# Performance work log

Hardware: AMD Instinct MI355X
Metric: run time of the kernel (lower is better)

Reference implementation:

```python
import jax, jax.numpy as jnp
import numpy as np

B, T = 8192, 2048


def setup_inputs() -> dict:
    key = jax.random.key(0)
    u = jax.random.normal(key, (B, T, 1), dtype=jnp.float32)
    return {
        "u": u,
        "dt": jnp.float32(0.01),
        "m": jnp.float32(1.0),
        "c": jnp.float32(0.1),
        "k": jnp.float32(2.0),
        "in_mean": jnp.float32(0.5),
        "in_std": jnp.float32(2.0),
        "out_mean": jnp.float32(0.0),
        "out_std": jnp.float32(1.5),
    }


def reference(u, dt, m, c, k, in_mean, in_std, out_mean, out_std):
    # u: (B, T, 1) scaled forcing signal; state: (B, 2) = [position, velocity]
    Bsz = u.shape[0]
    u_seq = jnp.transpose(u[..., 0])  # (T, B) for lax.scan over time
    state0 = jnp.zeros((Bsz, 2), dtype=u.dtype)

    def step(state, u_t):
        # in_s.inverse_transform: unscale input
        u_p = u_t * in_std + in_mean  # (B,)
        x, v = state[:, 0], state[:, 1]
        # prior(state, u_p): mass-spring-damper derivative [dx, dv]
        acc = (u_p - c * v - k * x) / m
        new_state = state + dt * jnp.stack([v, acc], axis=1)  # Euler step
        # prior.ay on the UPDATED state (matches torch: state updated first)
        ay = (u_p - c * new_state[:, 1] - k * new_state[:, 0]) / m
        # out_s.transform: scale output
        y = (ay - out_mean) / out_std  # (B,)
        return new_state, y

    state_T, ys = jax.lax.scan(step, state0, u_seq)  # ys: (T, B)
    return jnp.transpose(ys), state_T  # (B, T), (B, 2)
```

## Files before the change

kernel.cpp:

```cpp
#include <hip/hip_runtime.h>

#define TT 2048
#define LP 32

__device__ __forceinline__ float b2f(unsigned short h) {
    union { unsigned int u; float f; } x; x.u = ((unsigned int)h) << 16; return x.f;
}
__device__ __forceinline__ unsigned short f2b(float f) {
    union { float f; unsigned int u; } x; x.f = f;
    unsigned int r = x.u + 0x7fffu + ((x.u >> 16) & 1u);
    return (unsigned short)(r >> 16);
}
__device__ __forceinline__ float ldsc(const void* p, bool bf) {
    return bf ? b2f(*(const unsigned short*)p) : *(const float*)p;
}

__global__ __launch_bounds__(256, 4) void phys_scan(
    const void* __restrict__ u_in,
    const void* __restrict__ p_dt, const void* __restrict__ p_m,
    const void* __restrict__ p_c,  const void* __restrict__ p_k,
    const void* __restrict__ p_im, const void* __restrict__ p_is,
    const void* __restrict__ p_om, const void* __restrict__ p_os,
    void* __restrict__ out, int rows)
{
    const int lane = threadIdx.x & 63;
    const int b = blockIdx.x * 4 + (threadIdx.x >> 6);
    if (b >= rows) return;

    const bool bf = (((const unsigned short*)p_m)[0] != 0);

    const float dt = ldsc(p_dt, bf);
    const float mm = ldsc(p_m,  bf);
    const float cc = ldsc(p_c,  bf);
    const float kk = ldsc(p_k,  bf);
    const float im = ldsc(p_im, bf);
    const float is = ldsc(p_is, bf);
    const float om = ldsc(p_om, bf);
    const float os = ldsc(p_os, bf);

    const float inv_m  = 1.0f / mm;
    const float inv_os = 1.0f / os;
    const float a21 = -dt * kk * inv_m;
    const float a22 = 1.0f - dt * cc * inv_m;
    const float dtm = dt * inv_m;

    const size_t base = (size_t)b * TT + (size_t)lane * LP;

    float uf[LP];
    if (bf) {
        const uint4* p = (const uint4*)((const unsigned short*)u_in + base);
        #pragma unroll
        for (int i = 0; i < 4; i++) {
            uint4 w = p[i];
            unsigned int ws[4] = {w.x, w.y, w.z, w.w};
            #pragma unroll
            for (int j = 0; j < 4; j++) {
                uf[i*8 + j*2 + 0] = b2f((unsigned short)(ws[j] & 0xffffu));
                uf[i*8 + j*2 + 1] = b2f((unsigned short)(ws[j] >> 16));
            }
        }
    } else {
        const float4* p = (const float4*)((const float*)u_in + base);
        #pragma unroll
        for (int i = 0; i < 8; i++) {
            float4 w = p[i];
            uf[i*4+0]=w.x; uf[i*4+1]=w.y; uf[i*4+2]=w.z; uf[i*4+3]=w.w;
        }
    }

    float px = 0.f, pv = 0.f;
    #pragma unroll
    for (int i = 0; i < LP; i++) {
        float up = uf[i] * is + im;
        uf[i] = up;
        float nx = px + dt * pv;
        float nv = a21 * px + a22 * pv + dtm * up;
        px = nx; pv = nv;
    }

    float m00 = 1.f, m01 = dt, m10 = a21, m11 = a22;
    #pragma unroll
    for (int i = 0; i < 5; i++) {
        float t00 = m00*m00 + m01*m10;
        float t01 = m00*m01 + m01*m11;
        float t10 = m10*m00 + m11*m10;
        float t11 = m10*m01 + m11*m11;
        m00=t00; m01=t01; m10=t10; m11=t11;
    }

    #pragma unroll
    for (int o = 1; o < 64; o <<= 1) {
        float rx = __shfl_up(px, o, 64);
        float rv = __shfl_up(pv, o, 64);
        if (lane >= o) {
            px = m00*rx + m01*rv + px;
            pv = m10*rx + m11*rv + pv;
        }
        if (o < 32) {
            float t00 = m00*m00 + m01*m10;
            float t01 = m00*m01 + m01*m11;
            float t10 = m10*m00 + m11*m10;
            float t11 = m10*m01 + m11*m11;
            m00=t00; m01=t01; m10=t10; m11=t11;
        }
    }

    float ex = __shfl_up(px, 1, 64);
    float ev = __shfl_up(pv, 1, 64);
    if (lane == 0) { ex = 0.f; ev = 0.f; }

    float x = ex, v = ev;
    #pragma unroll
    for (int i = 0; i < LP; i++) {
        float up = uf[i];
        float nx = x + dt * v;
        float nv = a21 * x + a22 * v + dtm * up;
        float ay = (up - cc * nv - kk * nx) * inv_m;
        uf[i] = (ay - om) * inv_os;
        x = nx; v = nv;
    }

    if (bf) {
        unsigned short* ob = (unsigned short*)out;
        uint4* p = (uint4*)(ob + base);
        #pragma unroll
        for (int i = 0; i < 4; i++) {
            uint4 w;
            w.x = (unsigned)f2b(uf[i*8+0]) | ((unsigned)f2b(uf[i*8+1]) << 16);
            w.y = (unsigned)f2b(uf[i*8+2]) | ((unsigned)f2b(uf[i*8+3]) << 16);
            w.z = (unsigned)f2b(uf[i*8+4]) | ((unsigned)f2b(uf[i*8+5]) << 16);
            w.w = (unsigned)f2b(uf[i*8+6]) | ((unsigned)f2b(uf[i*8+7]) << 16);
            p[i] = w;
        }
        if (lane == 63) {
            size_t so = (size_t)rows * TT + (size_t)b * 2;
            ob[so]   = f2b(px);
            ob[so+1] = f2b(pv);
        }
    } else {
        float* of = (float*)out;
        float4* p = (float4*)(of + base);
        #pragma unroll
        for (int i = 0; i < 8; i++) {
            p[i] = make_float4(uf[i*4+0], uf[i*4+1], uf[i*4+2], uf[i*4+3]);
        }
        if (lane == 63) {
            size_t so = (size_t)rows * TT + (size_t)b * 2;
            of[so]   = px;
            of[so+1] = pv;
        }
    }
}

extern "C" void kernel_launch(void* const* d_in, const int* in_sizes, int n_in,
                              void* d_out, int out_size, void* d_ws, size_t ws_size,
                              hipStream_t stream) {
    const int rows = in_sizes[0] / TT;
    const int blocks = (rows + 3) / 4;
    hipLaunchKernelGGL(phys_scan, dim3(blocks), dim3(256), 0, stream,
                       d_in[0], d_in[1], d_in[2], d_in[3], d_in[4],
                       d_in[5], d_in[6], d_in[7], d_in[8],
                       d_out, rows);
}
```

Measured before the change: 140.0 us.

## Process each row in coalesced wave-wide segments with carried scan state

Each row is now handled as a sequence of 1 KB segments, one 16-byte chunk per lane per segment, instead of 32 contiguous elements per lane. Loads and stores across the wave therefore become fully coalesced, and the next segment is prefetched while the current one is computed. The state carried between segments is propagated with precomputed transition-matrix powers, and dtype branches are split into templates. In exchange there are more shuffle-scan passes per row (one per segment), which adds cross-lane work and latency.

```diff
diff --git a/kernel.cpp b/kernel.cpp
--- a/kernel.cpp
+++ b/kernel.cpp
@@ -1,7 +1,6 @@
 #include <hip/hip_runtime.h>
 
 #define TT 2048
-#define LP 32
 
 __device__ __forceinline__ float b2f(unsigned short h) {
     union { unsigned int u; float f; } x; x.u = ((unsigned int)h) << 16; return x.f;
@@ -13,6 +12,149 @@
 }
 __device__ __forceinline__ float ldsc(const void* p, bool bf) {
     return bf ? b2f(*(const unsigned short*)p) : *(const float*)p;
+}
+
+template<bool BF>
+__device__ void run_row(
+    const void* __restrict__ u_in, void* __restrict__ out,
+    int rows, int b, int lane,
+    float dt, float cc, float kk, float inv_m,
+    float im, float is, float om, float inv_os)
+{
+    constexpr int LPS  = BF ? 8 : 4;
+    constexpr int NSEG = BF ? 4 : 8;
+    constexpr int ES   = BF ? 2 : 4;
+
+    const float a21 = -dt * kk * inv_m;
+    const float a22 = 1.0f - dt * cc * inv_m;
+    const float dtm = dt * inv_m;
+
+    float L[6][4];
+    {
+        float m00 = 1.f, m01 = dt, m10 = a21, m11 = a22;
+        constexpr int SQ = BF ? 3 : 2;
+        #pragma unroll
+        for (int i = 0; i < SQ; i++) {
+            float t00=m00*m00+m01*m10, t01=m00*m01+m01*m11;
+            float t10=m10*m00+m11*m10, t11=m10*m01+m11*m11;
+            m00=t00; m01=t01; m10=t10; m11=t11;
+        }
+        #pragma unroll
+        for (int k = 0; k < 6; k++) {
+            L[k][0]=m00; L[k][1]=m01; L[k][2]=m10; L[k][3]=m11;
+            float t00=m00*m00+m01*m10, t01=m00*m01+m01*m11;
+            float t10=m10*m00+m11*m10, t11=m10*m01+m11*m11;
+            m00=t00; m01=t01; m10=t10; m11=t11;
+        }
+    }
+    float w00 = 1.f, w01 = 0.f, w10 = 0.f, w11 = 1.f;
+    #pragma unroll
+    for (int k = 0; k < 6; k++) {
+        if ((lane >> k) & 1) {
+            float t00 = L[k][0]*w00 + L[k][1]*w10;
+            float t01 = L[k][0]*w01 + L[k][1]*w11;
+            float t10 = L[k][2]*w00 + L[k][3]*w10;
+            float t11 = L[k][2]*w01 + L[k][3]*w11;
+            w00=t00; w01=t01; w10=t10; w11=t11;
+        }
+    }
+
+    const char* gin  = (const char*)u_in + (size_t)b * TT * ES;
+    char*       gout = (char*)out        + (size_t)b * TT * ES;
+
+    float cx = 0.f, cv = 0.f;
+
+    uint4 cur = *(const uint4*)(gin + (size_t)lane * 16);
+
+    #pragma unroll
+    for (int seg = 0; seg < NSEG; seg++) {
+        uint4 nxt = cur;
+        if (seg + 1 < NSEG)
+            nxt = *(const uint4*)(gin + (size_t)(seg + 1) * 1024 + (size_t)lane * 16);
+
+        float uf[LPS];
+        if (BF) {
+            unsigned int ws[4] = {cur.x, cur.y, cur.z, cur.w};
+            #pragma unroll
+            for (int q = 0; q < 4; q++) {
+                uf[q*2 + 0] = b2f((unsigned short)(ws[q] & 0xffffu));
+                uf[q*2 + 1] = b2f((unsigned short)(ws[q] >> 16));
+            }
+        } else {
+            uf[0] = __uint_as_float(cur.x);
+            uf[1] = __uint_as_float(cur.y);
+            uf[2] = __uint_as_float(cur.z);
+            uf[3] = __uint_as_float(cur.w);
+        }
+
+        float px = 0.f, pv = 0.f;
+        #pragma unroll
+        for (int i = 0; i < LPS; i++) {
+            float up = uf[i] * is + im;
+            uf[i] = up;
+            float nx = px + dt * pv;
+            float nv = a21 * px + a22 * pv + dtm * up;
+            px = nx; pv = nv;
+        }
+
+        #pragma unroll
+        for (int k = 0; k < 6; k++) {
+            float rx = __shfl_up(px, 1 << k, 64);
+            float rv = __shfl_up(pv, 1 << k, 64);
+            if (lane >= (1 << k)) {
+                px = L[k][0]*rx + L[k][1]*rv + px;
+                pv = L[k][2]*rx + L[k][3]*rv + pv;
+            }
+        }
+
+        float ex = __shfl_up(px, 1, 64);
+        float ev = __shfl_up(pv, 1, 64);
+        if (lane == 0) { ex = 0.f; ev = 0.f; }
+        float x = w00*cx + w01*cv + ex;
+        float v = w10*cx + w11*cv + ev;
+
+        #pragma unroll
+        for (int i = 0; i < LPS; i++) {
+            float up = uf[i];
+            float nx = x + dt * v;
+            float nv = a21 * x + a22 * v + dtm * up;
+            float ay = (up - cc * nv - kk * nx) * inv_m;
+            uf[i] = (ay - om) * inv_os;
+            x = nx; v = nv;
+        }
+
+        cx = __shfl(x, 63, 64);
+        cv = __shfl(v, 63, 64);
+
+        uint4 o;
+        if (BF) {
+            o.x = (unsigned)f2b(uf[0]) | ((unsigned)f2b(uf[1]) << 16);
+            o.y = (unsigned)f2b(uf[2]) | ((unsigned)f2b(uf[3]) << 16);
+            o.z = (unsigned)f2b(uf[4]) | ((unsigned)f2b(uf[5]) << 16);
+            o.w = (unsigned)f2b(uf[6]) | ((unsigned)f2b(uf[7]) << 16);
+        } else {
+            o.x = __float_as_uint(uf[0]);
+            o.y = __float_as_uint(uf[1]);
+            o.z = __float_as_uint(uf[2]);
+            o.w = __float_as_uint(uf[3]);
+        }
+        *(uint4*)(gout + (size_t)seg * 1024 + (size_t)lane * 16) = o;
+
+        cur = nxt;
+    }
+
+    if (lane == 0) {
+        if (BF) {
+            unsigned short* ob = (unsigned short*)out;
+            size_t so = (size_t)rows * TT + (size_t)b * 2;
+            *(unsigned int*)(ob + so) =
+                (unsigned)f2b(cx) | ((unsigned)f2b(cv) << 16);
+        } else {
+            float* of = (float*)out;
+            size_t so = (size_t)rows * TT + (size_t)b * 2;
+            *(float2*)(of + so) = make_float2(cx, cv);
+        }
+    }
 }
 
 __global__ __launch_bounds__(256, 4) void phys_scan(
@@ -37,119 +179,13 @@
     const float is = ldsc(p_is, bf);
     const float om = ldsc(p_om, bf);
     const float os = ldsc(p_os, bf);
-
     const float inv_m  = 1.0f / mm;
     const float inv_os = 1.0f / os;
-    const float a21 = -dt * kk * inv_m;
-    const float a22 = 1.0f - dt * cc * inv_m;
-    const float dtm = dt * inv_m;
-
-    const size_t base = (size_t)b * TT + (size_t)lane * LP;
-
-    float uf[LP];
-    if (bf) {
-        const uint4* p = (const uint4*)((const unsigned short*)u_in + base);
-        #pragma unroll
-        for (int i = 0; i < 4; i++) {
-            uint4 w = p[i];
-            unsigned int ws[4] = {w.x, w.y, w.z, w.w};
-            #pragma unroll
-            for (int j = 0; j < 4; j++) {
-                uf[i*8 + j*2 + 0] = b2f((unsigned short)(ws[j] & 0xffffu));
-                uf[i*8 + j*2 + 1] = b2f((unsigned short)(ws[j] >> 16));
-            }
-        }
-    } else {
-        const float4* p = (const float4*)((const float*)u_in + base);
-        #pragma unroll
-        for (int i = 0; i < 8; i++) {
-            float4 w = p[i];
-            uf[i*4+0]=w.x; uf[i*4+1]=w.y; uf[i*4+2]=w.z; uf[i*4+3]=w.w;
-        }
-    }
-
-    float px = 0.f, pv = 0.f;
-    #pragma unroll
-    for (int i = 0; i < LP; i++) {
-        float up = uf[i] * is + im;
-        uf[i] = up;
-        float nx = px + dt * pv;
-        float nv = a21 * px + a22 * pv + dtm * up;
-        px = nx; pv = nv;
-    }
-
-    float m00 = 1.f, m01 = dt, m10 = a21, m11 = a22;
-    #pragma unroll
-    for (int i = 0; i < 5; i++) {
-        float t00 = m00*m00 + m01*m10;
-        float t01 = m00*m01 + m01*m11;
-        float t10 = m10*m00 + m11*m10;
-        float t11 = m10*m01 + m11*m11;
-        m00=t00; m01=t01; m10=t10; m11=t11;
-    }
-
-    #pragma unroll
-    for (int o = 1; o < 64; o <<= 1) {
-        float rx = __shfl_up(px, o, 64);
-        float rv = __shfl_up(pv, o, 64);
-        if (lane >= o) {
-            px = m00*rx + m01*rv + px;
-            pv = m10*rx + m11*rv + pv;
-        }
-        if (o < 32) {
-            float t00 = m00*m00 + m01*m10;
-            float t01 = m00*m01 + m01*m11;
-            float t10 = m10*m00 + m11*m10;
-            float t11 = m10*m01 + m11*m11;
-            m00=t00; m01=t01; m10=t10; m11=t11;
-        }
-    }
-
-    float ex = __shfl_up(px, 1, 64);
-    float ev = __shfl_up(pv, 1, 64);
-    if (lane == 0) { ex = 0.f; ev = 0.f; }
-
-    float x = ex, v = ev;
-    #pragma unroll
-    for (int i = 0; i < LP; i++) {
-        float up = uf[i];
-        float nx = x + dt * v;
-        float nv = a21 * x + a22 * v + dtm * up;
-        float ay = (up - cc * nv - kk * nx) * inv_m;
-        uf[i] = (ay - om) * inv_os;
-        x = nx; v = nv;
-    }
-
-    if (bf) {
-        unsigned short* ob = (unsigned short*)out;
-        uint4* p = (uint4*)(ob + base);
-        #pragma unroll
-        for (int i = 0; i < 4; i++) {
-            uint4 w;
-            w.x = (unsigned)f2b(uf[i*8+0]) | ((unsigned)f2b(uf[i*8+1]) << 16);
-            w.y = (unsigned)f2b(uf[i*8+2]) | ((unsigned)f2b(uf[i*8+3]) << 16);
-            w.z = (unsigned)f2b(uf[i*8+4]) | ((unsigned)f2b(uf[i*8+5]) << 16);
-            w.w = (unsigned)f2b(uf[i*8+6]) | ((unsigned)f2b(uf[i*8+7]) << 16);
-            p[i] = w;
-        }
-        if (lane == 63) {
-            size_t so = (size_t)rows * TT + (size_t)b * 2;
-            ob[so]   = f2b(px);
-            ob[so+1] = f2b(pv);
-        }
-    } else {
-        float* of = (float*)out;
-        float4* p = (float4*)(of + base);
-        #pragma unroll
-        for (int i = 0; i < 8; i++) {
-            p[i] = make_float4(uf[i*4+0], uf[i*4+1], uf[i*4+2], uf[i*4+3]);
-        }
-        if (lane == 63) {
-            size_t so = (size_t)rows * TT + (size_t)b * 2;
-            of[so]   = px;
-            of[so+1] = pv;
-        }
-    }
+
+    if (bf) run_row<true >(u_in, out, rows, b, lane,
+                           dt, cc, kk, inv_m, im, is, om, inv_os);
+    else    run_row<false>(u_in, out, rows, b, lane,
+                           dt, cc, kk, inv_m, im, is, om, inv_os);
 }
 
 extern "C" void kernel_launch(void* const* d_in, const int* in_sizes, int n_in,
```

Measured after the change: 137.8 us. About the same (-1.6%).
